# Optimization experiments

Measured on AMD Instinct MI355X. Metric: run time of the kernel, lower is better.

## Reference

```python
import jax, jax.numpy as jnp
import numpy as np

ALPHA = 0.05
GDEP = 2


def conv1x1(x, w, b):
    # x: [N,C,V,L], w: [O,C], b: [O]
    return jnp.einsum('ncvl,oc->novl', x, w) + b[None, :, None, None]


def setup_inputs() -> dict:
    key = jax.random.key(0)
    ks = jax.random.split(key, 9)
    N, C, V, L = 32, 32, 400, 12
    c_out = 32
    cat = (GDEP + 1) * C
    s = 0.05
    return {
        'x': jax.random.normal(ks[0], (N, C, V, L), jnp.float32),
        'w_lin1': jax.random.normal(ks[1], (C, C), jnp.float32) * s,
        'b_lin1': jnp.zeros((C,), jnp.float32),
        'w_lin2': jax.random.normal(ks[2], (C, C), jnp.float32) * s,
        'b_lin2': jnp.zeros((C,), jnp.float32),
        'w_mlp1': jax.random.normal(ks[3], (c_out, cat), jnp.float32) * s,
        'b_mlp1': jnp.zeros((c_out,), jnp.float32),
        'w_mlp2': jax.random.normal(ks[4], (c_out, cat), jnp.float32) * s,
        'b_mlp2': jnp.zeros((c_out,), jnp.float32),
    }


def reference(x, w_lin1, b_lin1, w_lin2, b_lin2, w_mlp1, b_mlp1, w_mlp2, b_mlp2):
    # dynamic adjacency: adj[n,v,w,l] = sum_c x1[n,c,v,l] * x2[n,c,w,l]
    x1 = jnp.tanh(conv1x1(x, w_lin1, b_lin1))
    x2 = jnp.tanh(conv1x1(x, w_lin2, b_lin2))
    adj = jnp.einsum('ncvl,ncwl->nvwl', x1, x2)  # [N,V,V,L]
    adj0 = jax.nn.softmax(adj, axis=2)
    adj1 = jax.nn.softmax(jnp.swapaxes(adj, 1, 2), axis=2)

    def diffuse(a):
        h = x
        out = [h]
        for _ in range(GDEP):
            # nconv: h[n,c,w,l] = sum_v h[n,c,v,l] * a[n,v,w,l]
            h = ALPHA * x + (1.0 - ALPHA) * jnp.einsum('ncvl,nvwl->ncwl', h, a)
            out.append(h)
        return jnp.concatenate(out, axis=1)  # [N,(GDEP+1)*C,V,L]

    ho1 = conv1x1(diffuse(adj0), w_mlp1, b_mlp1)
    ho2 = conv1x1(diffuse(adj1), w_mlp2, b_mlp2)
    return ho1 + ho2
```

## Files before the change

kernel.cpp:

```cpp
#include <hip/hip_runtime.h>
#include <stdint.h>

#define TT 1024
#define AL 0.05f
#define OM 0.95f
#define STRD 408
#define LOG2E 1.4426950408889634f

typedef short s4v __attribute__((ext_vector_type(4)));
typedef short s8v __attribute__((ext_vector_type(8)));
typedef float f4v __attribute__((ext_vector_type(4)));
typedef float f16v __attribute__((ext_vector_type(16)));
typedef int   i2v __attribute__((ext_vector_type(2)));

#define MF32(a,b,c) __builtin_amdgcn_mfma_f32_32x32x16_bf16(a,b,c,0,0,0)
#define MF16(a,b,c) __builtin_amdgcn_mfma_f32_16x16x32_bf16(a,b,c,0,0,0)

#if __has_builtin(__builtin_amdgcn_exp2f)
#define E2(x) __builtin_amdgcn_exp2f(x)
#else
#define E2(x) exp2f(x)
#endif

__device__ __forceinline__ uint16_t f2bf(float f){ union{float f;uint32_t i;}t; t.f=f; return (uint16_t)((t.i + 0x7fffu + ((t.i>>16)&1u))>>16); }
__device__ __forceinline__ float bf2f(uint16_t h){ union{uint32_t i;float f;}t; t.i=((uint32_t)h)<<16; return t.f; }
__device__ __forceinline__ float bfLO(uint32_t u){ union{uint32_t i;float f;}t; t.i=u<<16; return t.f; }
__device__ __forceinline__ float bfHI(uint32_t u){ union{uint32_t i;float f;}t; t.i=u&0xffff0000u; return t.f; }
__device__ __forceinline__ uint32_t cvtpk(float lo, float hi){ uint32_t r; asm("v_cvt_pk_bf16_f32 %0, %1, %2" : "=v"(r) : "v"(lo), "v"(hi)); return r; }
__device__ __forceinline__ void pl32swap(uint32_t &x, uint32_t &y){
#if __has_builtin(__builtin_amdgcn_permlane32_swap)
  i2v rr = __builtin_amdgcn_permlane32_swap((int)x, (int)y, false, false);
  x = (uint32_t)rr.x; y = (uint32_t)rr.y;
#else
  asm("v_permlane32_swap_b32 %0, %1" : "+v"(x), "+v"(y));
#endif
}
__device__ __forceinline__ float ftanh(float x){ float t = E2(2.885390081777927f*x); return __builtin_fmaf(-2.f, __builtin_amdgcn_rcpf(1.f + t), 1.f); }
__device__ __forceinline__ s8v ld8(const uint16_t* p){ return *(const s8v*)p; }
__device__ __forceinline__ s8v ld8u(const uint16_t* p){
  s4v lo = *(const s4v*)p; s4v hi = *(const s4v*)(p+4);
  return __builtin_shufflevector(lo, hi, 0,1,2,3,4,5,6,7);
}
#define ROWF(e2) (((e2)&3) + 8*((e2)>>2) + 4*h2)
#define VXA(row,off) ((((row)<<5) + (off)) ^ (((row)&7)<<3))

__device__ __align__(16) float gStage[32*12*12800];

#define X1S 0
#define X2S 12800
#define XCV 25600
#define PBA 38656
#define HCV 54656
#define GCV 67712
#define RINV 80768
#define CINV 81168

__global__ __launch_bounds__(TT) void dymix(
    const float* __restrict__ x,
    const float* __restrict__ w1, const float* __restrict__ b1,
    const float* __restrict__ w2, const float* __restrict__ b2,
    const float* __restrict__ wm1, const float* __restrict__ bm1,
    const float* __restrict__ wm2, const float* __restrict__ bm2)
{
  __shared__ __align__(16) uint16_t S[81568];

  const int blk = blockIdx.x;
  const int xcd = blk & 7, slot = blk >> 3;
  const int n = xcd*4 + slot/12;
  const int l = slot - (slot/12)*12;
  const int t = threadIdx.x;
  const int wv = t >> 6;
  const int lane = t & 63;
  const int q  = lane >> 4;
  const int r  = lane & 15;
  const int h2 = lane >> 5;
  const int m32 = lane & 31;
  const long xbase = (long)n*153600 + l;

  for (int i = t; i < 12800; i += TT) {
    int c = i / 400, v = i - c*400;
    S[XCV + c*STRD + v] = f2bf(x[xbase + (long)i*12]);
  }
  __syncthreads();

  for (int i = t; i < 12800; i += TT) { int v = i>>5, c = i&31; S[PBA + VXA(v,c)] = S[XCV + c*STRD + v]; }
  for (int i = t; i < 1024; i += TT) {
    int o = i>>5, c = i&31;
    S[PBA + 12800 + o*40 + c] = f2bf(w1[i]);
    S[PBA + 14080 + o*40 + c] = f2bf(w2[i]);
  }
  if (t < 32) { ((float*)(S+PBA+15360))[t] = b1[t]; ((float*)(S+PBA+15424))[t] = b2[t]; }
  __syncthreads();

  #pragma unroll
  for (int j = 0; j < 2; ++j) {
    int u = wv + 16*j;
    if (u < 24) {
      int nt = u >> 1, li = u & 1;
      const uint16_t* W = S + PBA + 12800 + li*1280;
      const float* bfp = (const float*)(S + PBA + 15360 + li*64);
      uint16_t* dst = S + (li ? X2S : X1S);
      const float osc = li ? 1.f : LOG2E;
      f16v z = {};
      #pragma unroll
      for (int kk = 0; kk < 2; ++kk) {
        s8v a = ld8(W + m32*40 + kk*16 + h2*8);
        s8v b = ld8(S + PBA + VXA(nt*32 + m32, kk*16 + h2*8));
        z = MF32(a, b, z);
      }
      int v = nt*32 + m32;
      #pragma unroll
      for (int g = 0; g < 4; ++g) {
        float p0 = ftanh(z[4*g+0] + bfp[8*g+4*h2+0]) * osc;
        float p1 = ftanh(z[4*g+1] + bfp[8*g+4*h2+1]) * osc;
        float p2 = ftanh(z[4*g+2] + bfp[8*g+4*h2+2]) * osc;
        float p3 = ftanh(z[4*g+3] + bfp[8*g+4*h2+3]) * osc;
        uint2 d; d.x = cvtpk(p0,p1); d.y = cvtpk(p2,p3);
        *(uint2*)(dst + VXA(v, 8*g + 4*h2)) = d;
      }
    } else if (u < 28) {
      int li = (u-24)>>1, mt = u&1;
      const uint16_t* W = S + PBA + 12800 + li*1280;
      const float* bfp = (const float*)(S + PBA + 15360 + li*64);
      uint16_t* dst = S + (li ? X2S : X1S);
      const float osc = li ? 1.f : LOG2E;
      s8v a = ld8(W + (mt*16 + r)*40 + q*8);
      s8v b = ld8(S + PBA + VXA(384 + r, q*8));
      f4v z4 = {}; z4 = MF16(a, b, z4);
      float p0 = ftanh(z4[0] + bfp[mt*16+q*4+0]) * osc;
      float p1 = ftanh(z4[1] + bfp[mt*16+q*4+1]) * osc;
      float p2 = ftanh(z4[2] + bfp[mt*16+q*4+2]) * osc;
      float p3 = ftanh(z4[3] + bfp[mt*16+q*4+3]) * osc;
      uint2 d; d.x = cvtpk(p0,p1); d.y = cvtpk(p2,p3);
      *(uint2*)(dst + VXA(384 + r, mt*16 + q*4)) = d;
    }
  }
  s8v xf0, xf1, xft;
  {
    int m0 = (wv < 12) ? wv : 0;
    xf0 = ld8(S + PBA + VXA(m0*32 + m32, h2*8));
    xf1 = ld8(S + PBA + VXA(m0*32 + m32, 16 + h2*8));
    xft = ld8(S + PBA + VXA(384 + r, q*8));
  }
  __syncthreads();

  float* rsf = (float*)(S + HCV);
  float* csf = rsf + 400;
  for (int i = t; i < 400; i += TT) csf[i] = 0.f;
  __syncthreads();
  {
    s8v av[2]; f4v rac[2] = {{},{}};
    #pragma unroll
    for (int jj = 0; jj < 2; ++jj) { int vt = wv + 16*jj; if (vt < 25) av[jj] = ld8(S + X1S + VXA(vt*16 + r, q*8)); }
    for (int wt = 0; wt < 25; ++wt) {
      s8v b = ld8(S + X2S + VXA(wt*16 + r, q*8));
      float cp = 0.f;
      #pragma unroll
      for (int jj = 0; jj < 2; ++jj) {
        int vt = wv + 16*jj;
        if (vt < 25) {
          f4v z = {}; z = MF16(av[jj], b, z);
          #pragma unroll
          for (int e = 0; e < 4; ++e) { float ev = E2(z[e]); rac[jj][e] += ev; cp += ev; }
        }
      }
      cp += __shfl_xor(cp, 16); cp += __shfl_xor(cp, 32);
      if (q == 0) atomicAdd(&csf[wt*16 + r], cp);
    }
    #pragma unroll
    for (int jj = 0; jj < 2; ++jj) {
      int vt = wv + 16*jj;
      if (vt < 25) {
        #pragma unroll
        for (int e = 0; e < 4; ++e) {
          float s = rac[jj][e];
          s += __shfl_xor(s,1); s += __shfl_xor(s,2); s += __shfl_xor(s,4); s += __shfl_xor(s,8);
          if (r == 0) rsf[vt*16 + q*4 + e] = s;
        }
      }
    }
  }
  __syncthreads();
  for (int i = t; i < 400; i += TT) { S[RINV + i] = f2bf(1.f/rsf[i]); S[CINV + i] = f2bf(1.f/csf[i]); }
  __syncthreads();

  f16v acc[2];
  for (int step = 0; step < 2; ++step) {
    { f16v zv = {}; acc[0]=zv; acc[1]=zv; }
    const uint16_t* AH = S + (step ? HCV : XCV);
    const uint16_t* AG = S + (step ? GCV : XCV);
    uint16_t* P0 = S + (step ? 40256 : PBA);
    uint16_t* P1 = S + (step ? XCV : 53056);
    for (int sb = 0; sb < 13; ++sb) {
      const int vbase = sb*32;
      const bool lastsb = (sb == 12);
      const int kmax = lastsb ? 1 : 2;
      s8v fr[2][2];
      #pragma unroll
      for (int jj = 0; jj < 2; ++jj) {
        int g = wv + 16*jj;
        if (g >= 26) continue;
        int chain = (g < 13) ? 0 : 1;
        int uu = g - 13*chain;
        const uint16_t* sa = S + (chain ? X2S : X1S);
        const uint16_t* sb2 = S + (chain ? X1S : X2S);
        const int scl = chain ? CINV : RINV;
        if (uu < 12) {
          s8v a0 = ld8(sa + VXA(vbase + m32, h2*8));
          s8v a1 = ld8(sa + VXA(vbase + m32, 16 + h2*8));
          s8v b0 = ld8(sb2 + VXA(uu*32 + m32, h2*8));
          s8v b1 = ld8(sb2 + VXA(uu*32 + m32, 16 + h2*8));
          f16v z = {}; z = MF32(a0, b0, z); z = MF32(a1, b1, z);
          #pragma unroll
          for (int k = 0; k < 2; ++k) {
            if (k < kmax) {
              const uint16_t* spt = S + scl + vbase + 16*k + 4*h2;
              uint32_t sAB = *(const uint32_t*)(spt);
              uint32_t sCD = *(const uint32_t*)(spt + 2);
              uint32_t sEF = *(const uint32_t*)(spt + 8);
              uint32_t sGH = *(const uint32_t*)(spt + 10);
              uint32_t C0 = cvtpk(E2(z[8*k+0])*bfLO(sAB), E2(z[8*k+1])*bfHI(sAB));
              uint32_t C1 = cvtpk(E2(z[8*k+2])*bfLO(sCD), E2(z[8*k+3])*bfHI(sCD));
              uint32_t C2 = cvtpk(E2(z[8*k+4])*bfLO(sEF), E2(z[8*k+5])*bfHI(sEF));
              uint32_t C3 = cvtpk(E2(z[8*k+6])*bfLO(sGH), E2(z[8*k+7])*bfHI(sGH));
              pl32swap(C0, C2);
              pl32swap(C1, C3);
              union { uint32_t d[4]; s8v v8; } F;
              F.d[0] = C0; F.d[1] = C1; F.d[2] = C2; F.d[3] = C3;
              fr[jj][k] = F.v8;
            }
          }
        } else {
          uint16_t* P = chain ? P1 : P0;
          int ctmax = lastsb ? 1 : 2;
          for (int ct = 0; ct < ctmax; ++ct) {
            s8v a = ld8(sa + VXA(vbase + ct*16 + r, q*8));
            s8v b = ld8(sb2 + VXA(384 + r, q*8));
            f4v z4 = {}; z4 = MF16(a, b, z4);
            float p0 = E2(z4[0]) * bf2f(S[scl + vbase + ct*16 + q*4 + 0]);
            float p1 = E2(z4[1]) * bf2f(S[scl + vbase + ct*16 + q*4 + 1]);
            float p2 = E2(z4[2]) * bf2f(S[scl + vbase + ct*16 + q*4 + 2]);
            float p3 = E2(z4[3]) * bf2f(S[scl + vbase + ct*16 + q*4 + 3]);
            uint2 d; d.x = cvtpk(p0,p1); d.y = cvtpk(p2,p3);
            *(uint2*)(P + (384 + r)*36 + ct*16 + q*4) = d;
          }
          if (lastsb && lane < 16) {
            uint2 z0 = {0u,0u};
            uint16_t* pz = P + (384 + lane)*36 + 16;
            *(uint2*)(pz) = z0; *(uint2*)(pz+4) = z0; *(uint2*)(pz+8) = z0; *(uint2*)(pz+12) = z0;
          }
        }
      }
      #pragma unroll
      for (int jj = 0; jj < 2; ++jj) {
        int g = wv + 16*jj;
        if (g >= 26) continue;
        int chain = (g < 13) ? 0 : 1;
        int uu = g - 13*chain;
        const uint16_t* Acv = chain ? AG : AH;
        if (uu < 12) {
          #pragma unroll
          for (int k = 0; k < 2; ++k) {
            if (k < kmax) {
              s8v a = ld8(Acv + m32*STRD + vbase + k*16 + h2*8);
              acc[jj] = MF32(a, fr[jj][k], acc[jj]);
            }
          }
        } else {
          uint16_t* P = chain ? P1 : P0;
          #pragma unroll
          for (int mt2 = 0; mt2 < 2; ++mt2) {
            int koff = (lastsb && q >= 2) ? 0 : q*8;
            s8v a = ld8(Acv + (mt2*16 + r)*STRD + vbase + koff);
            s8v b = ld8u(P + (384 + r)*36 + q*8);
            f4v c4 = { acc[jj][4*mt2+0], acc[jj][4*mt2+1], acc[jj][4*mt2+2], acc[jj][4*mt2+3] };
            c4 = MF16(a, b, c4);
            acc[jj][4*mt2+0]=c4[0]; acc[jj][4*mt2+1]=c4[1]; acc[jj][4*mt2+2]=c4[2]; acc[jj][4*mt2+3]=c4[3];
          }
        }
      }
    }
    __syncthreads();
    if (step == 0) {
      #pragma unroll
      for (int jj = 0; jj < 2; ++jj) {
        int g = wv + 16*jj;
        if (g >= 26) continue;
        int chain = (g < 13) ? 0 : 1;
        int uu = g - 13*chain;
        uint16_t* dst = S + (chain ? GCV : HCV);
        if (uu < 12) {
          int w = uu*32 + m32;
          #pragma unroll
          for (int e2 = 0; e2 < 16; ++e2) {
            int c = ROWF(e2);
            dst[c*STRD + w] = f2bf(AL*bf2f(S[XCV + c*STRD + w]) + OM*acc[jj][e2]);
          }
        } else {
          int w = 384 + r;
          #pragma unroll
          for (int mt2 = 0; mt2 < 2; ++mt2)
            #pragma unroll
            for (int e = 0; e < 4; ++e) {
              int c = mt2*16 + q*4 + e;
              dst[c*STRD + w] = f2bf(AL*bf2f(S[XCV + c*STRD + w]) + OM*acc[jj][4*mt2+e]);
            }
        }
      }
      __syncthreads();
    }
  }

  for (int i = t; i < 12800; i += TT) {
    int v = i >> 5, c = i & 31;
    int d = VXA(v, c);
    S[X1S + d] = S[HCV + c*STRD + v];
    S[X2S + d] = S[GCV + c*STRD + v];
  }
  #pragma unroll
  for (int jj = 0; jj < 2; ++jj) {
    int g = wv + 16*jj;
    if (g >= 26) continue;
    int chain = (g < 13) ? 0 : 1;
    int uu = g - 13*chain;
    uint16_t* dst = S + (chain ? PBA : XCV);
    if (uu < 12) {
      int w = uu*32 + m32;
      #pragma unroll
      for (int gg = 0; gg < 4; ++gg) {
        uint2 d;
        d.x = cvtpk(OM*acc[jj][4*gg+0], OM*acc[jj][4*gg+1]);
        d.y = cvtpk(OM*acc[jj][4*gg+2], OM*acc[jj][4*gg+3]);
        *(uint2*)(dst + VXA(w, 8*gg + 4*h2)) = d;
      }
    } else {
      int w = 384 + r;
      #pragma unroll
      for (int mt2 = 0; mt2 < 2; ++mt2) {
        uint2 d;
        d.x = cvtpk(OM*acc[jj][4*mt2+0], OM*acc[jj][4*mt2+1]);
        d.y = cvtpk(OM*acc[jj][4*mt2+2], OM*acc[jj][4*mt2+3]);
        *(uint2*)(dst + VXA(w, mt2*16 + q*4)) = d;
      }
    }
  }
  __syncthreads();
  for (int i = t; i < 1024; i += TT) {
    int o = i >> 5, c = i & 31;
    float h2w = wm1[o*96 + 64 + c], g2w = wm2[o*96 + 64 + c];
    S[HCV +        o*40 + c] = f2bf(wm1[o*96 + c] + wm2[o*96 + c] + AL*(h2w + g2w));
    S[HCV + 1280 + o*40 + c] = f2bf(wm1[o*96 + 32 + c]);
    S[HCV + 2560 + o*40 + c] = f2bf(h2w);
    S[HCV + 3840 + o*40 + c] = f2bf(wm2[o*96 + 32 + c]);
    S[HCV + 5120 + o*40 + c] = f2bf(g2w);
  }
  if (t < 32) ((float*)(S + HCV + 6400))[t] = bm1[t] + bm2[t];
  __syncthreads();

  {
    const float* boF = (const float*)(S + HCV + 6400);
    float* oSl = gStage + (long)(n*12 + l)*12800;
    const int fb[5] = { 0, X1S, XCV, X2S, PBA };
    int m = wv;
    if (m < 12) {
      f16v z = {};
      #pragma unroll
      for (int p = 0; p < 5; ++p) {
        #pragma unroll
        for (int kk = 0; kk < 2; ++kk) {
          s8v a = ld8(S + HCV + p*1280 + m32*40 + kk*16 + h2*8);
          s8v b;
          if (p == 0) b = kk ? xf1 : xf0;
          else        b = ld8(S + fb[p] + VXA(m*32 + m32, kk*16 + h2*8));
          z = MF32(a, b, z);
        }
      }
      int v = m*32 + m32;
      #pragma unroll
      for (int e2 = 0; e2 < 16; ++e2) {
        int o = ROWF(e2);
        oSl[o*400 + v] = z[e2] + boF[o];
      }
    } else if (m < 14) {
      int mt = m - 12;
      f4v z4 = {};
      #pragma unroll
      for (int p = 0; p < 5; ++p) {
        s8v a = ld8(S + HCV + p*1280 + (mt*16 + r)*40 + q*8);
        s8v b = (p == 0) ? xft : ld8(S + fb[p] + VXA(384 + r, q*8));
        z4 = MF16(a, b, z4);
      }
      #pragma unroll
      for (int e = 0; e < 4; ++e) {
        int o = mt*16 + q*4 + e;
        oSl[o*400 + 384 + r] = z4[e] + boF[o];
      }
    }
  }
}

__global__ __launch_bounds__(256) void finT(float* __restrict__ out) {
  int idx = blockIdx.x*256 + threadIdx.x;
  int n = idx / 12800, ov = idx - n*12800;
  const float* src = gStage + (long)n*153600 + ov;
  float vals[12];
  #pragma unroll
  for (int l = 0; l < 12; ++l) vals[l] = src[(long)l*12800];
  float4* dst = (float4*)(out + (long)idx*12);
  dst[0] = make_float4(vals[0],vals[1],vals[2],vals[3]);
  dst[1] = make_float4(vals[4],vals[5],vals[6],vals[7]);
  dst[2] = make_float4(vals[8],vals[9],vals[10],vals[11]);
}

extern "C" void kernel_launch(void* const* d_in, const int* in_sizes, int n_in,
                              void* d_out, int out_size, void* d_ws, size_t ws_size,
                              hipStream_t stream) {
  (void)in_sizes; (void)n_in; (void)out_size; (void)d_ws; (void)ws_size;
  dymix<<<dim3(384), dim3(TT), 0, stream>>>(
      (const float*)d_in[0],
      (const float*)d_in[1], (const float*)d_in[2],
      (const float*)d_in[3], (const float*)d_in[4],
      (const float*)d_in[5], (const float*)d_in[6],
      (const float*)d_in[7], (const float*)d_in[8]);
  finT<<<dim3(1600), dim3(256), 0, stream>>>((float*)d_out);
}
```

Baseline: 235.8 us.

## Software-pipeline LDS operand loads and hoist loop-invariant B fragments in diffusion loop

Hoists the loop-invariant B fragments (hb0/hb1) out of the step and sb loops, and prefetches the next iteration's A-operand, diffusion-input and scale values from LDS into registers one iteration ahead. It also prefetches the next x2 fragment in the column-sum loop, adds launch_bounds minimum-blocks 4, and raises wave priority around the accumulate MFMAs with s_setprio. The aim is to hide LDS latency behind the MFMA and exp work. The trade-off is higher register pressure from double-buffered fragments, which could cause spills at 1024 threads.

New measurement: 774.4 us. 3.28x slower.

```diff
diff --git a/kernel.cpp b/kernel.cpp
--- a/kernel.cpp
+++ b/kernel.cpp
@@ -55,7 +55,7 @@
 #define RINV 80768
 #define CINV 81168
 
-__global__ __launch_bounds__(TT) void dymix(
+__global__ __launch_bounds__(TT, 4) void dymix(
     const float* __restrict__ x,
     const float* __restrict__ w1, const float* __restrict__ b1,
     const float* __restrict__ w2, const float* __restrict__ b2,
@@ -152,8 +152,10 @@
     s8v av[2]; f4v rac[2] = {{},{}};
     #pragma unroll
     for (int jj = 0; jj < 2; ++jj) { int vt = wv + 16*jj; if (vt < 25) av[jj] = ld8(S + X1S + VXA(vt*16 + r, q*8)); }
+    s8v bnx = ld8(S + X2S + VXA(r, q*8));
     for (int wt = 0; wt < 25; ++wt) {
-      s8v b = ld8(S + X2S + VXA(wt*16 + r, q*8));
+      s8v b = bnx;
+      if (wt < 24) bnx = ld8(S + X2S + VXA((wt+1)*16 + r, q*8));
       float cp = 0.f;
       #pragma unroll
       for (int jj = 0; jj < 2; ++jj) {
@@ -184,6 +186,24 @@
   for (int i = t; i < 400; i += TT) { S[RINV + i] = f2bf(1.f/rsf[i]); S[CINV + i] = f2bf(1.f/csf[i]); }
   __syncthreads();
 
+  bool act_[2]; int ch_[2], uu_[2]; bool mn_[2];
+  const uint16_t *saB[2], *sbB[2]; int sclB[2];
+  #pragma unroll
+  for (int jj = 0; jj < 2; ++jj) {
+    int g = wv + 16*jj; act_[jj] = (g < 26);
+    int ch = (g < 13) ? 0 : 1; ch_[jj] = ch; int u = g - 13*ch; uu_[jj] = u; mn_[jj] = (u < 12);
+    saB[jj] = S + (ch ? X2S : X1S);
+    sbB[jj] = S + (ch ? X1S : X2S);
+    sclB[jj] = ch ? CINV : RINV;
+  }
+  s8v hb0[2], hb1[2];
+  #pragma unroll
+  for (int jj = 0; jj < 2; ++jj) {
+    if (!act_[jj]) continue;
+    if (mn_[jj]) { hb0[jj] = ld8(sbB[jj] + VXA(uu_[jj]*32 + m32, h2*8)); hb1[jj] = ld8(sbB[jj] + VXA(uu_[jj]*32 + m32, 16 + h2*8)); }
+    else          hb0[jj] = ld8(sbB[jj] + VXA(384 + r, q*8));
+  }
+
   f16v acc[2];
   for (int step = 0; step < 2; ++step) {
     { f16v zv = {}; acc[0]=zv; acc[1]=zv; }
@@ -191,34 +211,52 @@
     const uint16_t* AG = S + (step ? GCV : XCV);
     uint16_t* P0 = S + (step ? 40256 : PBA);
     uint16_t* P1 = S + (step ? XCV : 53056);
+    const uint16_t* Acv[2]; uint16_t* Pp[2];
+    #pragma unroll
+    for (int jj = 0; jj < 2; ++jj) { Acv[jj] = ch_[jj] ? AG : AH; Pp[jj] = ch_[jj] ? P1 : P0; }
+
+    s8v ta0[2], ta1[2], gA0[2], gA1[2]; uint2 s01[2][2], s23[2][2];
+    #pragma unroll
+    for (int jj = 0; jj < 2; ++jj) {
+      if (!(act_[jj] && mn_[jj])) continue;
+      ta0[jj] = ld8(saB[jj] + VXA(m32, h2*8));
+      ta1[jj] = ld8(saB[jj] + VXA(m32, 16 + h2*8));
+      gA0[jj] = ld8(Acv[jj] + m32*STRD + h2*8);
+      gA1[jj] = ld8(Acv[jj] + m32*STRD + 16 + h2*8);
+      const uint16_t* sp = S + sclB[jj] + 4*h2;
+      s01[jj][0] = *(const uint2*)(sp);      s23[jj][0] = *(const uint2*)(sp + 8);
+      s01[jj][1] = *(const uint2*)(sp + 16); s23[jj][1] = *(const uint2*)(sp + 24);
+    }
+    #pragma unroll 2
     for (int sb = 0; sb < 13; ++sb) {
       const int vbase = sb*32;
       const bool lastsb = (sb == 12);
       const int kmax = lastsb ? 1 : 2;
+      s8v nta0[2], nta1[2], ngA0[2], ngA1[2]; uint2 ns01[2][2], ns23[2][2];
+      if (!lastsb) {
+        const int nvb = vbase + 32;
+        #pragma unroll
+        for (int jj = 0; jj < 2; ++jj) {
+          if (!(act_[jj] && mn_[jj])) continue;
+          nta0[jj] = ld8(saB[jj] + VXA(nvb + m32, h2*8));
+          nta1[jj] = ld8(saB[jj] + VXA(nvb + m32, 16 + h2*8));
+          ngA0[jj] = ld8(Acv[jj] + m32*STRD + nvb + h2*8);
+          ngA1[jj] = ld8(Acv[jj] + m32*STRD + nvb + 16 + h2*8);
+          const uint16_t* sp = S + sclB[jj] + nvb + 4*h2;
+          ns01[jj][0] = *(const uint2*)(sp);      ns23[jj][0] = *(const uint2*)(sp + 8);
+          ns01[jj][1] = *(const uint2*)(sp + 16); ns23[jj][1] = *(const uint2*)(sp + 24);
+        }
+      }
       s8v fr[2][2];
       #pragma unroll
       for (int jj = 0; jj < 2; ++jj) {
-        int g = wv + 16*jj;
-        if (g >= 26) continue;
-        int chain = (g < 13) ? 0 : 1;
-        int uu = g - 13*chain;
-        const uint16_t* sa = S + (chain ? X2S : X1S);
-        const uint16_t* sb2 = S + (chain ? X1S : X2S);
-        const int scl = chain ? CINV : RINV;
-        if (uu < 12) {
-          s8v a0 = ld8(sa + VXA(vbase + m32, h2*8));
-          s8v a1 = ld8(sa + VXA(vbase + m32, 16 + h2*8));
-          s8v b0 = ld8(sb2 + VXA(uu*32 + m32, h2*8));
-          s8v b1 = ld8(sb2 + VXA(uu*32 + m32, 16 + h2*8));
-          f16v z = {}; z = MF32(a0, b0, z); z = MF32(a1, b1, z);
+        if (!act_[jj]) continue;
+        if (mn_[jj]) {
+          f16v z = {}; z = MF32(ta0[jj], hb0[jj], z); z = MF32(ta1[jj], hb1[jj], z);
           #pragma unroll
           for (int k = 0; k < 2; ++k) {
             if (k < kmax) {
-              const uint16_t* spt = S + scl + vbase + 16*k + 4*h2;
-              uint32_t sAB = *(const uint32_t*)(spt);
-              uint32_t sCD = *(const uint32_t*)(spt + 2);
-              uint32_t sEF = *(const uint32_t*)(spt + 8);
-              uint32_t sGH = *(const uint32_t*)(spt + 10);
+              uint32_t sAB = s01[jj][k].x, sCD = s01[jj][k].y, sEF = s23[jj][k].x, sGH = s23[jj][k].y;
               uint32_t C0 = cvtpk(E2(z[8*k+0])*bfLO(sAB), E2(z[8*k+1])*bfHI(sAB));
               uint32_t C1 = cvtpk(E2(z[8*k+2])*bfLO(sCD), E2(z[8*k+3])*bfHI(sCD));
               uint32_t C2 = cvtpk(E2(z[8*k+4])*bfLO(sEF), E2(z[8*k+5])*bfHI(sEF));
@@ -231,12 +269,12 @@
             }
           }
         } else {
-          uint16_t* P = chain ? P1 : P0;
+          uint16_t* P = Pp[jj];
+          const int scl = sclB[jj];
           int ctmax = lastsb ? 1 : 2;
           for (int ct = 0; ct < ctmax; ++ct) {
-            s8v a = ld8(sa + VXA(vbase + ct*16 + r, q*8));
-            s8v b = ld8(sb2 + VXA(384 + r, q*8));
-            f4v z4 = {}; z4 = MF16(a, b, z4);
+            s8v a = ld8(saB[jj] + VXA(vbase + ct*16 + r, q*8));
+            f4v z4 = {}; z4 = MF16(a, hb0[jj], z4);
             float p0 = E2(z4[0]) * bf2f(S[scl + vbase + ct*16 + q*4 + 0]);
             float p1 = E2(z4[1]) * bf2f(S[scl + vbase + ct*16 + q*4 + 1]);
             float p2 = E2(z4[2]) * bf2f(S[scl + vbase + ct*16 + q*4 + 2]);
@@ -251,27 +289,20 @@
           }
         }
       }
+      __builtin_amdgcn_s_setprio(1);
       #pragma unroll
       for (int jj = 0; jj < 2; ++jj) {
-        int g = wv + 16*jj;
-        if (g >= 26) continue;
-        int chain = (g < 13) ? 0 : 1;
-        int uu = g - 13*chain;
-        const uint16_t* Acv = chain ? AG : AH;
-        if (uu < 12) {
-          #pragma unroll
-          for (int k = 0; k < 2; ++k) {
-            if (k < kmax) {
-              s8v a = ld8(Acv + m32*STRD + vbase + k*16 + h2*8);
-              acc[jj] = MF32(a, fr[jj][k], acc[jj]);
-            }
-          }
+        if (!act_[jj]) continue;
+        if (mn_[jj]) {
+          acc[jj] = MF32(gA0[jj], fr[jj][0], acc[jj]);
+          if (!lastsb) acc[jj] = MF32(gA1[jj], fr[jj][1], acc[jj]);
         } else {
-          uint16_t* P = chain ? P1 : P0;
+          uint16_t* P = Pp[jj];
+          const uint16_t* Ac = Acv[jj];
           #pragma unroll
           for (int mt2 = 0; mt2 < 2; ++mt2) {
             int koff = (lastsb && q >= 2) ? 0 : q*8;
-            s8v a = ld8(Acv + (mt2*16 + r)*STRD + vbase + koff);
+            s8v a = ld8(Ac + (mt2*16 + r)*STRD + vbase + koff);
             s8v b = ld8u(P + (384 + r)*36 + q*8);
             f4v c4 = { acc[jj][4*mt2+0], acc[jj][4*mt2+1], acc[jj][4*mt2+2], acc[jj][4*mt2+3] };
             c4 = MF16(a, b, c4);
@@ -279,18 +310,24 @@
           }
         }
       }
+      __builtin_amdgcn_s_setprio(0);
+      if (!lastsb) {
+        #pragma unroll
+        for (int jj = 0; jj < 2; ++jj) {
+          ta0[jj]=nta0[jj]; ta1[jj]=nta1[jj]; gA0[jj]=ngA0[jj]; gA1[jj]=ngA1[jj];
+          s01[jj][0]=ns01[jj][0]; s01[jj][1]=ns01[jj][1];
+          s23[jj][0]=ns23[jj][0]; s23[jj][1]=ns23[jj][1];
+        }
+      }
     }
     __syncthreads();
     if (step == 0) {
       #pragma unroll
       for (int jj = 0; jj < 2; ++jj) {
-        int g = wv + 16*jj;
-        if (g >= 26) continue;
-        int chain = (g < 13) ? 0 : 1;
-        int uu = g - 13*chain;
-        uint16_t* dst = S + (chain ? GCV : HCV);
-        if (uu < 12) {
-          int w = uu*32 + m32;
+        if (!act_[jj]) continue;
+        uint16_t* dst = S + (ch_[jj] ? GCV : HCV);
+        if (mn_[jj]) {
+          int w = uu_[jj]*32 + m32;
           #pragma unroll
           for (int e2 = 0; e2 < 16; ++e2) {
             int c = ROWF(e2);
@@ -319,13 +356,10 @@
   }
   #pragma unroll
   for (int jj = 0; jj < 2; ++jj) {
-    int g = wv + 16*jj;
-    if (g >= 26) continue;
-    int chain = (g < 13) ? 0 : 1;
-    int uu = g - 13*chain;
-    uint16_t* dst = S + (chain ? PBA : XCV);
-    if (uu < 12) {
-      int w = uu*32 + m32;
+    if (!act_[jj]) continue;
+    uint16_t* dst = S + (ch_[jj] ? PBA : XCV);
+    if (mn_[jj]) {
+      int w = uu_[jj]*32 + m32;
       #pragma unroll
       for (int gg = 0; gg < 4; ++gg) {
         uint2 d;
```

## Interchange diffusion loops per wave group, hoist invariant operand loads, prefetch adjacency tiles

Applied to the files above, without the earlier changes.

The diffusion step now runs the outer loop over each wave's job (jj) and the inner loop over source blocks, so the loop-invariant x2/x1 operand fragments are loaded once per job instead of once per source block. The special last partial block gets its own peeled path without kmax branches, and the accumulator stays in a local register variable. The row/column-sum loop also software-prefetches the next x2 tile. This trades lower LDS traffic and fewer branches for a changed instruction schedule and possibly higher register pressure from unroll 2.

Measured after the change: 254.2 us. 7.8% more time.

```diff
diff --git a/kernel.cpp b/kernel.cpp
--- a/kernel.cpp
+++ b/kernel.cpp
@@ -152,8 +152,10 @@
     s8v av[2]; f4v rac[2] = {{},{}};
     #pragma unroll
     for (int jj = 0; jj < 2; ++jj) { int vt = wv + 16*jj; if (vt < 25) av[jj] = ld8(S + X1S + VXA(vt*16 + r, q*8)); }
+    s8v bnx = ld8(S + X2S + VXA(r, q*8));
     for (int wt = 0; wt < 25; ++wt) {
-      s8v b = ld8(S + X2S + VXA(wt*16 + r, q*8));
+      s8v b = bnx;
+      if (wt < 24) bnx = ld8(S + X2S + VXA((wt+1)*16 + r, q*8));
       float cp = 0.f;
       #pragma unroll
       for (int jj = 0; jj < 2; ++jj) {
@@ -191,52 +193,78 @@
     const uint16_t* AG = S + (step ? GCV : XCV);
     uint16_t* P0 = S + (step ? 40256 : PBA);
     uint16_t* P1 = S + (step ? XCV : 53056);
-    for (int sb = 0; sb < 13; ++sb) {
-      const int vbase = sb*32;
-      const bool lastsb = (sb == 12);
-      const int kmax = lastsb ? 1 : 2;
-      s8v fr[2][2];
-      #pragma unroll
-      for (int jj = 0; jj < 2; ++jj) {
-        int g = wv + 16*jj;
-        if (g >= 26) continue;
-        int chain = (g < 13) ? 0 : 1;
-        int uu = g - 13*chain;
-        const uint16_t* sa = S + (chain ? X2S : X1S);
-        const uint16_t* sb2 = S + (chain ? X1S : X2S);
-        const int scl = chain ? CINV : RINV;
-        if (uu < 12) {
+    #pragma unroll
+    for (int jj = 0; jj < 2; ++jj) {
+      int g = wv + 16*jj;
+      if (g >= 26) continue;
+      int chain = (g < 13) ? 0 : 1;
+      int uu = g - 13*chain;
+      const uint16_t* sa = S + (chain ? X2S : X1S);
+      const uint16_t* sb2 = S + (chain ? X1S : X2S);
+      const int scl = chain ? CINV : RINV;
+      const uint16_t* Acv = chain ? AG : AH;
+      if (uu < 12) {
+        s8v hbA = ld8(sb2 + VXA(uu*32 + m32, h2*8));
+        s8v hbB = ld8(sb2 + VXA(uu*32 + m32, 16 + h2*8));
+        f16v av = acc[jj];
+        #pragma unroll 2
+        for (int sb = 0; sb < 12; ++sb) {
+          const int vbase = sb*32;
           s8v a0 = ld8(sa + VXA(vbase + m32, h2*8));
           s8v a1 = ld8(sa + VXA(vbase + m32, 16 + h2*8));
-          s8v b0 = ld8(sb2 + VXA(uu*32 + m32, h2*8));
-          s8v b1 = ld8(sb2 + VXA(uu*32 + m32, 16 + h2*8));
-          f16v z = {}; z = MF32(a0, b0, z); z = MF32(a1, b1, z);
+          f16v z = {}; z = MF32(a0, hbA, z); z = MF32(a1, hbB, z);
           #pragma unroll
           for (int k = 0; k < 2; ++k) {
-            if (k < kmax) {
-              const uint16_t* spt = S + scl + vbase + 16*k + 4*h2;
-              uint32_t sAB = *(const uint32_t*)(spt);
-              uint32_t sCD = *(const uint32_t*)(spt + 2);
-              uint32_t sEF = *(const uint32_t*)(spt + 8);
-              uint32_t sGH = *(const uint32_t*)(spt + 10);
-              uint32_t C0 = cvtpk(E2(z[8*k+0])*bfLO(sAB), E2(z[8*k+1])*bfHI(sAB));
-              uint32_t C1 = cvtpk(E2(z[8*k+2])*bfLO(sCD), E2(z[8*k+3])*bfHI(sCD));
-              uint32_t C2 = cvtpk(E2(z[8*k+4])*bfLO(sEF), E2(z[8*k+5])*bfHI(sEF));
-              uint32_t C3 = cvtpk(E2(z[8*k+6])*bfLO(sGH), E2(z[8*k+7])*bfHI(sGH));
-              pl32swap(C0, C2);
-              pl32swap(C1, C3);
-              union { uint32_t d[4]; s8v v8; } F;
-              F.d[0] = C0; F.d[1] = C1; F.d[2] = C2; F.d[3] = C3;
-              fr[jj][k] = F.v8;
-            }
+            const uint16_t* spt = S + scl + vbase + 16*k + 4*h2;
+            uint32_t sAB = *(const uint32_t*)(spt);
+            uint32_t sCD = *(const uint32_t*)(spt + 2);
+            uint32_t sEF = *(const uint32_t*)(spt + 8);
+            uint32_t sGH = *(const uint32_t*)(spt + 10);
+            uint32_t C0 = cvtpk(E2(z[8*k+0])*bfLO(sAB), E2(z[8*k+1])*bfHI(sAB));
+            uint32_t C1 = cvtpk(E2(z[8*k+2])*bfLO(sCD), E2(z[8*k+3])*bfHI(sCD));
+            uint32_t C2 = cvtpk(E2(z[8*k+4])*bfLO(sEF), E2(z[8*k+5])*bfHI(sEF));
+            uint32_t C3 = cvtpk(E2(z[8*k+6])*bfLO(sGH), E2(z[8*k+7])*bfHI(sGH));
+            pl32swap(C0, C2);
+            pl32swap(C1, C3);
+            union { uint32_t d[4]; s8v v8; } F;
+            F.d[0] = C0; F.d[1] = C1; F.d[2] = C2; F.d[3] = C3;
+            s8v ga = ld8(Acv + m32*STRD + vbase + k*16 + h2*8);
+            av = MF32(ga, F.v8, av);
           }
-        } else {
-          uint16_t* P = chain ? P1 : P0;
+        }
+        {
+          const int vbase = 384;
+          s8v a0 = ld8(sa + VXA(vbase + m32, h2*8));
+          s8v a1 = ld8(sa + VXA(vbase + m32, 16 + h2*8));
+          f16v z = {}; z = MF32(a0, hbA, z); z = MF32(a1, hbB, z);
+          const uint16_t* spt = S + scl + vbase + 4*h2;
+          uint32_t sAB = *(const uint32_t*)(spt);
+          uint32_t sCD = *(const uint32_t*)(spt + 2);
+          uint32_t sEF = *(const uint32_t*)(spt + 8);
+          uint32_t sGH = *(const uint32_t*)(spt + 10);
+          uint32_t C0 = cvtpk(E2(z[0])*bfLO(sAB), E2(z[1])*bfHI(sAB));
+          uint32_t C1 = cvtpk(E2(z[2])*bfLO(sCD), E2(z[3])*bfHI(sCD));
+          uint32_t C2 = cvtpk(E2(z[4])*bfLO(sEF), E2(z[5])*bfHI(sEF));
+          uint32_t C3 = cvtpk(E2(z[6])*bfLO(sGH), E2(z[7])*bfHI(sGH));
+          pl32swap(C0, C2);
+          pl32swap(C1, C3);
+          union { uint32_t d[4]; s8v v8; } F;
+          F.d[0] = C0; F.d[1] = C1; F.d[2] = C2; F.d[3] = C3;
+          s8v ga = ld8(Acv + m32*STRD + vbase + h2*8);
+          av = MF32(ga, F.v8, av);
+        }
+        acc[jj] = av;
+      } else {
+        uint16_t* P = chain ? P1 : P0;
+        s8v hbT = ld8(sb2 + VXA(384 + r, q*8));
+        f16v av = acc[jj];
+        for (int sb = 0; sb < 13; ++sb) {
+          const int vbase = sb*32;
+          const bool lastsb = (sb == 12);
           int ctmax = lastsb ? 1 : 2;
           for (int ct = 0; ct < ctmax; ++ct) {
             s8v a = ld8(sa + VXA(vbase + ct*16 + r, q*8));
-            s8v b = ld8(sb2 + VXA(384 + r, q*8));
-            f4v z4 = {}; z4 = MF16(a, b, z4);
+            f4v z4 = {}; z4 = MF16(a, hbT, z4);
             float p0 = E2(z4[0]) * bf2f(S[scl + vbase + ct*16 + q*4 + 0]);
             float p1 = E2(z4[1]) * bf2f(S[scl + vbase + ct*16 + q*4 + 1]);
             float p2 = E2(z4[2]) * bf2f(S[scl + vbase + ct*16 + q*4 + 2]);
@@ -249,35 +277,17 @@
             uint16_t* pz = P + (384 + lane)*36 + 16;
             *(uint2*)(pz) = z0; *(uint2*)(pz+4) = z0; *(uint2*)(pz+8) = z0; *(uint2*)(pz+12) = z0;
           }
-        }
-      }
-      #pragma unroll
-      for (int jj = 0; jj < 2; ++jj) {
-        int g = wv + 16*jj;
-        if (g >= 26) continue;
-        int chain = (g < 13) ? 0 : 1;
-        int uu = g - 13*chain;
-        const uint16_t* Acv = chain ? AG : AH;
-        if (uu < 12) {
-          #pragma unroll
-          for (int k = 0; k < 2; ++k) {
-            if (k < kmax) {
-              s8v a = ld8(Acv + m32*STRD + vbase + k*16 + h2*8);
-              acc[jj] = MF32(a, fr[jj][k], acc[jj]);
-            }
-          }
-        } else {
-          uint16_t* P = chain ? P1 : P0;
           #pragma unroll
           for (int mt2 = 0; mt2 < 2; ++mt2) {
             int koff = (lastsb && q >= 2) ? 0 : q*8;
             s8v a = ld8(Acv + (mt2*16 + r)*STRD + vbase + koff);
             s8v b = ld8u(P + (384 + r)*36 + q*8);
-            f4v c4 = { acc[jj][4*mt2+0], acc[jj][4*mt2+1], acc[jj][4*mt2+2], acc[jj][4*mt2+3] };
+            f4v c4 = { av[4*mt2+0], av[4*mt2+1], av[4*mt2+2], av[4*mt2+3] };
             c4 = MF16(a, b, c4);
-            acc[jj][4*mt2+0]=c4[0]; acc[jj][4*mt2+1]=c4[1]; acc[jj][4*mt2+2]=c4[2]; acc[jj][4*mt2+3]=c4[3];
+            av[4*mt2+0]=c4[0]; av[4*mt2+1]=c4[1]; av[4*mt2+2]=c4[2]; av[4*mt2+3]=c4[3];
           }
         }
+        acc[jj] = av;
       }
     }
     __syncthreads();
```
